# Kernel tuning notes

Measured on AMD Instinct MI355X. Metric: run time of the kernel, lower is better.

## Reference

```python
import jax, jax.numpy as jnp
import numpy as np


def setup_inputs() -> dict:
    key = jax.random.key(0)
    ks = jax.random.split(key, 9)
    B, T, S, E, H = 4, 4096, 4096, 512, 64
    return {
        "x": jax.random.normal(ks[0], (B, T, 1), dtype=jnp.float32),
        "tok_emb": jax.random.normal(ks[1], (B, S, E), dtype=jnp.float32),
        "key_w": jax.random.normal(ks[2], (H, E), dtype=jnp.float32) * 0.05,
        "key_b": jax.random.normal(ks[3], (H,), dtype=jnp.float32) * 0.05,
        "query_w": jax.random.normal(ks[4], (H, 1), dtype=jnp.float32) * 0.05,
        "query_b": jax.random.normal(ks[5], (H,), dtype=jnp.float32) * 0.05,
        "value_w": jax.random.normal(ks[6], (H, E), dtype=jnp.float32) * 0.05,
        "proj_w": jax.random.normal(ks[7], (1, H), dtype=jnp.float32) * 0.05,
        "proj_b": jax.random.normal(ks[8], (1,), dtype=jnp.float32) * 0.05,
    }


def reference(x, tok_emb, key_w, key_b, query_w, query_b, value_w, proj_w, proj_b):
    # k = tanh(Linear(tok_emb))            [B,S,H]
    k = jnp.tanh(jnp.einsum("bse,he->bsh", tok_emb, key_w) + key_b)
    # q = tanh(Linear(x)); x last dim is 1 [B,T,H]
    q = jnp.tanh(jnp.einsum("btu,hu->bth", x, query_w) + query_b)
    scale = k.shape[-1] ** (-0.5)
    wei = jnp.einsum("bth,bsh->bts", q, k) * scale  # [B,T,S]
    # NOTE: softmax over dim=-2 (the query/T axis), faithful to the original
    wei = jax.nn.softmax(wei, axis=-2)
    v = jnp.tanh(jnp.einsum("bse,he->bsh", tok_emb, value_w))  # [B,S,H]
    out = jnp.tanh(jnp.einsum("bts,bsh->bth", wei, v))         # [B,T,H]
    out = jnp.einsum("bth,oh->bto", out, proj_w) + proj_b      # [B,T,1]
    return jnp.squeeze(out, axis=-1)                            # [B,T]
```

## Files before the change

### kernel.cpp

```cpp
#include <hip/hip_runtime.h>
#include <math.h>

#define BB 4
#define TT 4096
#define SS 4096
#define EE 512
#define HH 64
#define NN 128
#define XR 6.0f


typedef __attribute__((ext_vector_type(8))) __bf16 bf16x8;
typedef __attribute__((ext_vector_type(16))) float f32x16;

__device__ __forceinline__ unsigned short f2b(float f) {
  unsigned int u = __float_as_uint(f);
  return (unsigned short)((u + 0x7FFFu + ((u >> 16) & 1u)) >> 16);
}

__device__ __forceinline__ float fast_tanh(float v) {
  float e = __expf(fminf(60.0f, 2.0f * v));
  return (e - 1.0f) * __builtin_amdgcn_rcpf(e + 1.0f);
}

__global__ __launch_bounds__(256) void prep_sm_kernel(
    const float* __restrict__ kw, const float* __restrict__ vw,
    const float* __restrict__ qw, const float* __restrict__ qb,
    const float* __restrict__ x, unsigned int* __restrict__ Wfrag,
    float* __restrict__ Cmat, unsigned short* __restrict__ qnA,
    float* __restrict__ Sm_part, float* __restrict__ Oz) {
  const int blk = blockIdx.x;
  if (blk < 64) {
    int idx = blk * 256 + threadIdx.x;
    int jq = idx & 1;
    int l = (idx >> 1) & 63;
    int ks = (idx >> 7) & 31;
    int nb = idx >> 12;
    int n = nb * 32 + (l & 31);
    int k = ks * 16 + (l >> 5) * 8 + jq * 4;
    const float* row = (n < HH) ? (kw + n * EE + k) : (vw + (n - HH) * EE + k);
    float4 wv = *(const float4*)row;
    Wfrag[idx * 2] = (unsigned int)f2b(wv.x) | ((unsigned int)f2b(wv.y) << 16);
    Wfrag[idx * 2 + 1] =
        (unsigned int)f2b(wv.z) | ((unsigned int)f2b(wv.w) << 16);
  } else if (blk < 128) {
    int idx = (blk - 64) * 256 + threadIdx.x;
    int m = idx >> 7;
    int j = idx & (NN - 1);
    Cmat[idx] = (float)cos((double)m * (M_PI * (j + 0.5) / NN));
    if (idx < 8192) ((float4*)Oz)[idx] = make_float4(0.f, 0.f, 0.f, 0.f);
  } else if (blk < 160) {
    int idx = (blk - 128) * 256 + threadIdx.x;
    int h = idx & 63;
    int j = idx >> 6;
    double th = M_PI * (j + 0.5) / NN;
    float xj = (float)(XR * cos(th));
    float val = tanhf(fmaf(xj, qw[h], qb[h]));
    int pos = (((j >> 5) * 4 + (h >> 4)) * 64 + (j & 31) + 32 * ((h >> 3) & 1)) * 8 +
              (h & 7);
    qnA[pos] = f2b(val);
  } else {
    __shared__ float Tm[128][NN + 1];
    int blk2 = blk - 160;
    int b = blk2 >> 5;
    int chunk = blk2 & 31;
    int tid = threadIdx.x;
    if (tid < 128) {
      float xh = x[b * TT + chunk * 128 + tid] * (1.0f / XR);
      xh = fminf(1.0f, fmaxf(-1.0f, xh));
      Tm[tid][0] = 1.0f;
      Tm[tid][1] = xh;
      float x2 = 2.0f * xh;
      float tm2 = 1.0f, tm1 = xh;
#pragma unroll 6
      for (int m = 2; m < NN; ++m) {
        float t = fmaf(x2, tm1, -tm2);
        Tm[tid][m] = t;
        tm2 = tm1;
        tm1 = t;
      }
    }
    __syncthreads();
    if (tid < 128) {
      float s = 0.f;
#pragma unroll 8
      for (int i = 0; i < 128; ++i) s += Tm[i][tid];
      Sm_part[(b * 32 + chunk) * NN + tid] = s;
    }
  }
}

__global__ __launch_bounds__(256) void kvattn_kernel(
    const float* __restrict__ emb, const float* __restrict__ kb,
    const unsigned int* __restrict__ Wfrag, const unsigned short* __restrict__ qnA,
    const float* __restrict__ Cmat, const float* __restrict__ Sm_part,
    float* __restrict__ O) {
  __shared__ __align__(16) char smem[69120];
  unsigned short* A_lds = (unsigned short*)smem;
  unsigned short* ktB = (unsigned short*)smem;
  unsigned short* vB = (unsigned short*)(smem + 8192);
  unsigned short* eA = (unsigned short*)(smem + 16384);
  float* zred = (float*)(smem + 65536);
  float* wql = (float*)(smem + 67840);
  float* izl = (float*)(smem + 68352);
  float* sml = (float*)(smem + 68608);

  const int tid = threadIdx.x;
  const int row0 = blockIdx.x * 64;
  const int bb = row0 >> 12;

#pragma unroll
  for (int mb = 0; mb < 2; ++mb) {
    int m = tid >> 3;
    int c8 = tid & 7;
    const float* src = emb + (size_t)(row0 + mb * 32 + m) * EE;
    unsigned short* dst = A_lds + mb * 16384;
#pragma unroll
    for (int it = 0; it < 16; ++it) {
      int k = (c8 + it * 8) * 4;
      float4 v = *(const float4*)(src + k);
      int kstep = k >> 4;
      int lane = m + 32 * ((k >> 3) & 1);
      int j = k & 7;
      unsigned int lo = (unsigned int)f2b(v.x) | ((unsigned int)f2b(v.y) << 16);
      unsigned int hi = (unsigned int)f2b(v.z) | ((unsigned int)f2b(v.w) << 16);
      *(uint2*)&dst[(kstep * 64 + lane) * 8 + j] = make_uint2(lo, hi);
    }
  }
  if (tid < 128) {
    float s = 0.f;
#pragma unroll 8
    for (int c = 0; c < 32; ++c) s += Sm_part[(bb * 32 + c) * NN + tid];
    sml[tid] = s;
  }
  __syncthreads();
  if (tid < 128) {
    float acc = sml[0] * (1.0f / NN);
    for (int m = 1; m < NN; ++m)
      acc = fmaf(sml[m] * (2.0f / NN), Cmat[m * NN + tid], acc);
    wql[tid] = acc;
  }

  const int w = tid >> 6;
  const int lane = tid & 63;
  f32x16 acc0 = {}, acc1 = {};
  const bf16x8* Bf = (const bf16x8*)Wfrag;
#pragma unroll 4
  for (int kstep = 0; kstep < 32; ++kstep) {
    bf16x8 bfr = Bf[(w * 32 + kstep) * 64 + lane];
    bf16x8 a0 = *(const bf16x8*)&A_lds[(kstep * 64 + lane) * 8];
    bf16x8 a1 = *(const bf16x8*)&A_lds[16384 + (kstep * 64 + lane) * 8];
    acc0 = __builtin_amdgcn_mfma_f32_32x32x16_bf16(a0, bfr, acc0, 0, 0, 0);
    acc1 = __builtin_amdgcn_mfma_f32_32x32x16_bf16(a1, bfr, acc1, 0, 0, 0);
  }
  __syncthreads();

  {
    const int n = w * 32 + (lane & 31);
    if (w < 2) {
      float kbv = kb[n];
      const int ks_h = n >> 4;
      const int off_h = 32 * ((n >> 3) & 1);
      const int jj_h = n & 7;
#pragma unroll
      for (int reg = 0; reg < 16; ++reg) {
        int sl = (reg & 3) + 8 * (reg >> 2) + 4 * (lane >> 5);
        ktB[(ks_h * 64 + sl + off_h) * 8 + jj_h] =
            f2b(fast_tanh(acc0[reg] + kbv));
        ktB[((4 + ks_h) * 64 + sl + off_h) * 8 + jj_h] =
            f2b(fast_tanh(acc1[reg] + kbv));
      }
    } else {
      int h = n - 64;
      const int nb_h = h >> 5;
      const int lm = h & 31;
#pragma unroll
      for (int reg = 0; reg < 16; ++reg) {
        int sl = (reg & 3) + 8 * (reg >> 2) + 4 * (lane >> 5);
        int s1 = sl + 32;
        vB[((nb_h * 4 + (sl >> 4)) * 64 + lm + 32 * ((sl >> 3) & 1)) * 8 +
           (sl & 7)] = f2b(fast_tanh(acc0[reg]));
        vB[((nb_h * 4 + (s1 >> 4)) * 64 + lm + 32 * ((s1 >> 3) & 1)) * 8 +
           (s1 & 7)] = f2b(fast_tanh(acc1[reg]));
      }
    }
  }
  __syncthreads();

  f32x16 l0 = {}, l1 = {};
#pragma unroll
  for (int ks = 0; ks < 4; ++ks) {
    bf16x8 a = *(const bf16x8*)(qnA + ((w * 4 + ks) * 64 + lane) * 8);
    bf16x8 b0 = *(const bf16x8*)&ktB[(ks * 64 + lane) * 8];
    bf16x8 b1 = *(const bf16x8*)&ktB[((4 + ks) * 64 + lane) * 8];
    l0 = __builtin_amdgcn_mfma_f32_32x32x16_bf16(a, b0, l0, 0, 0, 0);
    l1 = __builtin_amdgcn_mfma_f32_32x32x16_bf16(a, b1, l1, 0, 0, 0);
  }
  float e0[16], e1[16];
  float zp0 = 0.f, zp1 = 0.f;
#pragma unroll
  for (int r = 0; r < 4; ++r) {
    float4 wq4 = *(const float4*)&wql[w * 32 + 8 * r + 4 * (lane >> 5)];
    float wa[4] = {wq4.x, wq4.y, wq4.z, wq4.w};
#pragma unroll
    for (int c = 0; c < 4; ++c) {
      int reg = 4 * r + c;
      e0[reg] = __expf(l0[reg] * 0.125f);
      e1[reg] = __expf(l1[reg] * 0.125f);
      zp0 = fmaf(wa[c], e0[reg], zp0);
      zp1 = fmaf(wa[c], e1[reg], zp1);
    }
  }
  zred[(lane & 31) * 9 + w * 2 + (lane >> 5)] = zp0;
  zred[(32 + (lane & 31)) * 9 + w * 2 + (lane >> 5)] = zp1;
  __syncthreads();
  if (tid < 64) {
    float sum = 0.f;
#pragma unroll
    for (int k = 0; k < 8; ++k) sum += zred[tid * 9 + k];
    izl[tid] = 1.0f / sum;
  }
  __syncthreads();

  {
    const int sA = lane & 31, sB = 32 + (lane & 31);
    const float izA = izl[sA], izB = izl[sB];
    const int ksA = sA >> 4, oA = 32 * ((sA >> 3) & 1), jA = sA & 7;
    const int ksB = sB >> 4, oB = 32 * ((sB >> 3) & 1), jB = sB & 7;
#pragma unroll
    for (int reg = 0; reg < 16; ++reg) {
      int jl = (reg & 3) + 8 * (reg >> 2) + 4 * (lane >> 5);
      eA[((w * 4 + ksA) * 64 + jl + oA) * 8 + jA] = f2b(e0[reg] * izA);
      eA[((w * 4 + ksB) * 64 + jl + oB) * 8 + jB] = f2b(e1[reg] * izB);
    }
  }
  __syncthreads();
  f32x16 o0 = {}, o1 = {};
#pragma unroll
  for (int ks = 0; ks < 4; ++ks) {
    bf16x8 a = *(const bf16x8*)&eA[((w * 4 + ks) * 64 + lane) * 8];
    bf16x8 b0 = *(const bf16x8*)&vB[(ks * 64 + lane) * 8];
    bf16x8 b1 = *(const bf16x8*)&vB[((4 + ks) * 64 + lane) * 8];
    o0 = __builtin_amdgcn_mfma_f32_32x32x16_bf16(a, b0, o0, 0, 0, 0);
    o1 = __builtin_amdgcn_mfma_f32_32x32x16_bf16(a, b1, o1, 0, 0, 0);
  }
  float* op = O + (size_t)bb * (NN * HH);
  const int h0 = lane & 31, h1 = 32 + (lane & 31);
#pragma unroll
  for (int reg = 0; reg < 16; ++reg) {
    int j = w * 32 + (reg & 3) + 8 * (reg >> 2) + 4 * (lane >> 5);
    atomicAdd(&op[j * HH + h0], o0[reg]);
    atomicAdd(&op[j * HH + h1], o1[reg]);
  }
}

__global__ __launch_bounds__(256) void final_kernel(
    const float* __restrict__ x, const float* __restrict__ O,
    const float* __restrict__ pw, const float* __restrict__ pb,
    const float* __restrict__ Cmat, float* __restrict__ y) {
  const int idx = blockIdx.x * 256 + threadIdx.x;
  const int b = idx >> 12;
  __shared__ float yl[NN];
  __shared__ float c[NN];
  {
    const int j = threadIdx.x >> 1;
    const int half = threadIdx.x & 1;
    const float4* Ov =
        (const float4*)(O + ((size_t)(b * NN + j) * HH + half * 32));
    const float4* pwv = (const float4*)(pw + half * 32);
    float s = 0.f;
#pragma unroll
    for (int q = 0; q < 8; ++q) {
      float4 ov = Ov[q];
      float4 pv = pwv[q];
      s += fast_tanh(ov.x) * pv.x + fast_tanh(ov.y) * pv.y +
           fast_tanh(ov.z) * pv.z + fast_tanh(ov.w) * pv.w;
    }
    s += __shfl_xor(s, 1, 64);
    if (half == 0) yl[j] = s + pb[0];
  }
  __syncthreads();
  if (threadIdx.x < NN) {
    int m = threadIdx.x;
    double acc = 0.0;
#pragma unroll 8
    for (int j = 0; j < NN; ++j)
      acc += (double)yl[j] * (double)Cmat[m * NN + j];
    c[m] = (float)(acc * ((m == 0 ? 1.0 : 2.0) / NN));
  }
  __syncthreads();
  float xf = x[idx] * (1.0f / XR);
  xf = fminf(1.0f, fmaxf(-1.0f, xf));
  double xh = (double)xf;
  double b1 = 0.0, b2 = 0.0;
  for (int m = NN - 1; m >= 1; --m) {
    double t = fma(2.0 * xh, b1, (double)c[m] - b2);
    b2 = b1;
    b1 = t;
  }
  y[idx] = (float)fma(xh, b1, (double)c[0] - b2);
}

extern "C" void kernel_launch(void* const* d_in, const int* in_sizes, int n_in,
                              void* d_out, int out_size, void* d_ws,
                              size_t ws_size, hipStream_t stream) {
  const float* x = (const float*)d_in[0];
  const float* emb = (const float*)d_in[1];
  const float* kw = (const float*)d_in[2];
  const float* kb = (const float*)d_in[3];
  const float* qw = (const float*)d_in[4];
  const float* qb = (const float*)d_in[5];
  const float* vw = (const float*)d_in[6];
  const float* pw = (const float*)d_in[7];
  const float* pb = (const float*)d_in[8];

  float* ws = (float*)d_ws;
  float* O = ws;
  float* Cmat = ws + 32768;
  unsigned short* qnA = (unsigned short*)(Cmat + 16384);
  unsigned int* Wfrag = (unsigned int*)(Cmat + 16384 + 4096);
  float* Sm_part = (float*)(Wfrag + 32768);
  float* y = (float*)d_out;

  prep_sm_kernel<<<288, 256, 0, stream>>>(kw, vw, qw, qb, x, Wfrag, Cmat, qnA,
                                          Sm_part, O);
  kvattn_kernel<<<BB * SS / 64, 256, 0, stream>>>(emb, kb, Wfrag, qnA, Cmat,
                                                  Sm_part, O);
  final_kernel<<<BB * TT / 256, 256, 0, stream>>>(x, O, pw, pb, Cmat, y);
}
```

Before: 126.8 us.

## Drop double-precision cos in prep, batch embedding loads, split Chebyshev reduction chains

The Chebyshev cosine matrix is now built with single-precision cosf using integer angle reduction instead of double-precision cos. The qnA table setup is folded into the Cmat blocks, so the prep grid shrinks from 288 to 256 blocks. The embedding staging loop issues all 16 float4 loads before converting them, to raise memory-level parallelism. The per-row cosine reduction is split into four independent FMA chains with the weights prescaled. Together these trade some register pressure and float rounding for less FP64 work and shorter dependency chains.

```diff
diff --git a/kernel.cpp b/kernel.cpp
--- a/kernel.cpp
+++ b/kernel.cpp
@@ -47,21 +47,25 @@
     int idx = (blk - 64) * 256 + threadIdx.x;
     int m = idx >> 7;
     int j = idx & (NN - 1);
-    Cmat[idx] = (float)cos((double)m * (M_PI * (j + 0.5) / NN));
+    int k = (m * (2 * j + 1)) & 511;
+    if (k >= 256) k -= 512;
+    Cmat[idx] = cosf((float)k * (float)(M_PI / 256.0));
     if (idx < 8192) ((float4*)Oz)[idx] = make_float4(0.f, 0.f, 0.f, 0.f);
-  } else if (blk < 160) {
-    int idx = (blk - 128) * 256 + threadIdx.x;
-    int h = idx & 63;
-    int j = idx >> 6;
-    double th = M_PI * (j + 0.5) / NN;
-    float xj = (float)(XR * cos(th));
-    float val = tanhf(fmaf(xj, qw[h], qb[h]));
-    int pos = (((j >> 5) * 4 + (h >> 4)) * 64 + (j & 31) + 32 * ((h >> 3) & 1)) * 8 +
-              (h & 7);
-    qnA[pos] = f2b(val);
+    if (idx < 8192) {
+      int h = idx & 63;
+      int j2 = idx >> 6;
+      float th = (float)M_PI * ((float)j2 + 0.5f) * (1.0f / NN);
+      float xj = XR * cosf(th);
+      float val = tanhf(fmaf(xj, qw[h], qb[h]));
+      int pos =
+          (((j2 >> 5) * 4 + (h >> 4)) * 64 + (j2 & 31) + 32 * ((h >> 3) & 1)) *
+              8 +
+          (h & 7);
+      qnA[pos] = f2b(val);
+    }
   } else {
     __shared__ float Tm[128][NN + 1];
-    int blk2 = blk - 160;
+    int blk2 = blk - 128;
     int b = blk2 >> 5;
     int chunk = blk2 & 31;
     int tid = threadIdx.x;
@@ -115,10 +119,13 @@
     int c8 = tid & 7;
     const float* src = emb + (size_t)(row0 + mb * 32 + m) * EE;
     unsigned short* dst = A_lds + mb * 16384;
+    float4 buf[16];
+#pragma unroll
+    for (int it = 0; it < 16; ++it) buf[it] = *(const float4*)(src + (c8 + it * 8) * 4);
 #pragma unroll
     for (int it = 0; it < 16; ++it) {
       int k = (c8 + it * 8) * 4;
-      float4 v = *(const float4*)(src + k);
+      float4 v = buf[it];
       int kstep = k >> 4;
       int lane = m + 32 * ((k >> 3) & 1);
       int j = k & 7;
@@ -131,14 +138,19 @@
     float s = 0.f;
 #pragma unroll 8
     for (int c = 0; c < 32; ++c) s += Sm_part[(bb * 32 + c) * NN + tid];
-    sml[tid] = s;
+    sml[tid] = s * ((tid == 0) ? (1.0f / NN) : (2.0f / NN));
   }
   __syncthreads();
   if (tid < 128) {
-    float acc = sml[0] * (1.0f / NN);
-    for (int m = 1; m < NN; ++m)
-      acc = fmaf(sml[m] * (2.0f / NN), Cmat[m * NN + tid], acc);
-    wql[tid] = acc;
+    float a0 = 0.f, a1 = 0.f, a2 = 0.f, a3 = 0.f;
+#pragma unroll
+    for (int m = 0; m < NN; m += 4) {
+      a0 = fmaf(sml[m], Cmat[m * NN + tid], a0);
+      a1 = fmaf(sml[m + 1], Cmat[(m + 1) * NN + tid], a1);
+      a2 = fmaf(sml[m + 2], Cmat[(m + 2) * NN + tid], a2);
+      a3 = fmaf(sml[m + 3], Cmat[(m + 3) * NN + tid], a3);
+    }
+    wql[tid] = (a0 + a1) + (a2 + a3);
   }
 
   const int w = tid >> 6;
@@ -322,7 +334,7 @@
   float* Sm_part = (float*)(Wfrag + 32768);
   float* y = (float*)d_out;
 
-  prep_sm_kernel<<<288, 256, 0, stream>>>(kw, vw, qw, qb, x, Wfrag, Cmat, qnA,
+  prep_sm_kernel<<<256, 256, 0, stream>>>(kw, vw, qw, qb, x, Wfrag, Cmat, qnA,
                                           Sm_part, O);
   kvattn_kernel<<<BB * SS / 64, 256, 0, stream>>>(emb, kb, Wfrag, qnA, Cmat,
                                                   Sm_part, O);
```

Result: faster. 117.7 us (-7.2%).
